# Kernel optimization log

Hardware: AMD Instinct MI355X
Metric: run time of the kernel (lower is better)

## Reference

```python
import jax, jax.numpy as jnp
import numpy as np

SCALE = 100.0        # self.scale in the torch module
NUM_PIDS = 20000     # upper bound on particle_id values (fill_max)
N_HITS = 2_000_000
D_PARAMS = 8


def setup_inputs() -> dict:
    key = jax.random.key(0)
    ks = jax.random.split(key, 8)
    N, D = N_HITS, D_PARAMS
    return {
        "W": jax.random.uniform(ks[0], (N,), jnp.float32),
        "beta": jax.random.uniform(ks[1], (N,), jnp.float32, 1e-4, 1.0 - 1e-4),
        "H": jax.random.normal(ks[2], (N, D), jnp.float32),
        "pred": jax.random.normal(ks[3], (N, D), jnp.float32),
        "Y": jax.random.normal(ks[4], (N,), jnp.float32),
        "particle_id": jax.random.randint(ks[5], (N,), 0, NUM_PIDS, dtype=jnp.int32),
        "track_params": jax.random.normal(ks[6], (N, D), jnp.float32),
        "reconstructable": jnp.ones((N,), jnp.int32),
    }


def reference(W, beta, H, pred, Y, particle_id, track_params, reconstructable):
    # mask = reconstructable > 0; masked-out hits are routed to segment 0 (noise),
    # which is excluded from the per-pid loop, so math matches boolean indexing.
    valid = reconstructable > 0
    seg = jnp.where(valid, particle_id, 0)

    # MSE per hit: sum over param dim of squared error
    mse = jnp.sum(jnp.square(pred - track_params), axis=1)
    mse = jnp.where(valid, mse, 0.0)

    # In 'efficiency' mode the torch loop computes, per pid p:
    #   xi_p = M * p, weight = 1/sum(xi_p), contrib = weight * sum(mse * xi_p)
    #         = sum(mse * M) / count(M)   (the pid factor cancels exactly)
    # i.e. a segment-mean of mse over hits of each nonzero pid, averaged over pids.
    sums = jax.ops.segment_sum(mse, seg, num_segments=NUM_PIDS)
    counts = jax.ops.segment_sum(valid.astype(jnp.float32), seg, num_segments=NUM_PIDS)

    present = (counts > 0) & (jnp.arange(NUM_PIDS) > 0)  # pids from torch.unique(pid>0)
    per_pid_mean = jnp.where(present, sums / jnp.where(counts > 0, counts, 1.0), 0.0)
    K = jnp.sum(present.astype(jnp.float32))
    return SCALE * jnp.sum(per_pid_mean) / K
```

## Files before the change

kernel.cpp:

```cpp
#include <hip/hip_runtime.h>
#include <stdint.h>

#define NUM_PIDS 20000
#define HBLK_MAX 128
#define NCH      8
#define FIXB     512.0f
#define FXMASK   0x1FFFFu


__global__ void zero_acc_kernel(float* __restrict__ acc) {
    if (threadIdx.x < 2) acc[threadIdx.x] = 0.0f;
}

__global__ void __launch_bounds__(256) mse_kernel(
        const float4* __restrict__ pred,
        const float4* __restrict__ track,
        const int* __restrict__ pid,
        const int* __restrict__ recon,
        unsigned int* __restrict__ packed,
        int nf ) {
    int t = blockIdx.x * 256 + threadIdx.x;
    int stride = gridDim.x * 256;
    for (; t < nf; t += stride) {
        float4 a = pred[t], b = track[t];
        float d0 = a.x - b.x, d1 = a.y - b.y;
        float d2 = a.z - b.z, d3 = a.w - b.w;
        float part = d0*d0 + d1*d1 + d2*d2 + d3*d3;
        float mse = part + __shfl_xor(part, 1);
        int hit = t >> 1;
        int p = pid[hit];
        int r = recon[hit];
        unsigned int fx = (unsigned int)fminf(mse * FIXB + 0.5f, 131071.0f);
        unsigned int out = (p > 0 && r > 0) ? (((unsigned int)p << 17) | fx) : 0u;
        if ((t & 1) == 0) packed[hit] = out;
    }
}

__global__ void __launch_bounds__(1024) hist_kernel(
        const uint4* __restrict__ packed4,
        unsigned int* __restrict__ tbl,
        int n4,
        const unsigned int* __restrict__ packed,
        int n) {
    __shared__ unsigned int bins[NUM_PIDS];
    for (int j = threadIdx.x; j < NUM_PIDS; j += 1024) bins[j] = 0u;
    __syncthreads();
    int t = blockIdx.x * 1024 + threadIdx.x;
    int stride = gridDim.x * 1024;
    for (; t < n4; t += stride) {
        uint4 v = packed4[t];
        unsigned int p;
        p = v.x >> 17; if (p) atomicAdd(&bins[p], (1u << 24) | (v.x & FXMASK));
        p = v.y >> 17; if (p) atomicAdd(&bins[p], (1u << 24) | (v.y & FXMASK));
        p = v.z >> 17; if (p) atomicAdd(&bins[p], (1u << 24) | (v.z & FXMASK));
        p = v.w >> 17; if (p) atomicAdd(&bins[p], (1u << 24) | (v.w & FXMASK));
    }
    for (int i = 4 * n4 + blockIdx.x * 1024 + threadIdx.x; i < n; i += stride) {
        unsigned int c = packed[i];
        unsigned int p = c >> 17;
        if (p) atomicAdd(&bins[p], (1u << 24) | (c & FXMASK));
    }
    __syncthreads();
    unsigned int* my = tbl + (size_t)blockIdx.x * NUM_PIDS;
    for (int j = threadIdx.x; j < NUM_PIDS; j += 1024) my[j] = bins[j];
}

__global__ void __launch_bounds__(256) reduce1_kernel(
        const unsigned int* __restrict__ tbl,
        unsigned long long* __restrict__ tmp,
        int nblk) {
    int p = blockIdx.x * 256 + threadIdx.x;
    int c = blockIdx.y;
    if (p >= NUM_PIDS) return;
    int cs = (nblk + NCH - 1) / NCH;
    int b0 = c * cs, b1 = min(nblk, b0 + cs);
    unsigned long long sfx = 0ULL, cnt = 0ULL;
    for (int b = b0; b < b1; ++b) {
        unsigned int v = tbl[(size_t)b * NUM_PIDS + p];
        sfx += (unsigned long long)(v & 0xFFFFFFu);
        cnt += (unsigned long long)(v >> 24);
    }
    tmp[(size_t)c * NUM_PIDS + p] = (cnt << 40) | sfx;
}

__global__ void __launch_bounds__(256) reduce2_kernel(
        const unsigned long long* __restrict__ tmp,
        float* __restrict__ acc) {
    int p = blockIdx.x * 256 + threadIdx.x;
    float mean = 0.0f, pres = 0.0f;
    if (p >= 1 && p < NUM_PIDS) {
        unsigned long long s = 0ULL;
        #pragma unroll
        for (int c = 0; c < NCH; ++c) s += tmp[(size_t)c * NUM_PIDS + p];
        unsigned long long cnt = s >> 40;
        if (cnt > 0) {
            double sum = (double)(s & ((1ULL << 40) - 1)) * (1.0 / 512.0);
            mean = (float)(sum / (double)cnt);
            pres = 1.0f;
        }
    }
    #pragma unroll
    for (int off = 32; off > 0; off >>= 1) {
        mean += __shfl_down(mean, off);
        pres += __shfl_down(pres, off);
    }
    __shared__ float smean[4], spres[4];
    int wave = threadIdx.x >> 6, lane = threadIdx.x & 63;
    if (lane == 0) { smean[wave] = mean; spres[wave] = pres; }
    __syncthreads();
    if (threadIdx.x == 0) {
        atomicAdd(&acc[0], smean[0] + smean[1] + smean[2] + smean[3]);
        atomicAdd(&acc[1], spres[0] + spres[1] + spres[2] + spres[3]);
    }
}

__global__ void final_kernel(const float* __restrict__ acc,
                             float* __restrict__ out) {
    if (threadIdx.x == 0 && blockIdx.x == 0) {
        float K = acc[1];
        out[0] = (K > 0.0f) ? (100.0f * acc[0] / K) : 0.0f;
    }
}

extern "C" void kernel_launch(void* const* d_in, const int* in_sizes, int n_in,
                              void* d_out, int out_size, void* d_ws, size_t ws_size,
                              hipStream_t stream) {
    const float* pred  = (const float*)d_in[3];
    const int*   pid   = (const int*)d_in[5];
    const float* track = (const float*)d_in[6];
    const int*   recon = (const int*)d_in[7];
    int n = in_sizes[5];

    size_t packed_bytes = (((size_t)n * 4) + 63) & ~(size_t)63;
    size_t tmp_bytes = (size_t)NCH * NUM_PIDS * 8;
    int hblk = 8;
    if (ws_size > packed_bytes + tmp_bytes + 64 + (size_t)NUM_PIDS * 4) {
        size_t cap = (ws_size - packed_bytes - tmp_bytes - 64) / ((size_t)NUM_PIDS * 4);
        hblk = (int)(cap < HBLK_MAX ? cap : HBLK_MAX);
        if (hblk < 1) hblk = 1;
    }

    unsigned int* packed = (unsigned int*)d_ws;
    unsigned int* tbl = (unsigned int*)((char*)d_ws + packed_bytes);
    unsigned long long* tmp =
        (unsigned long long*)((char*)tbl + (size_t)hblk * NUM_PIDS * 4);
    float* acc = (float*)((char*)tmp + tmp_bytes);

    zero_acc_kernel<<<1, 64, 0, stream>>>(acc);
    mse_kernel<<<2048, 256, 0, stream>>>((const float4*)pred, (const float4*)track,
                                         pid, recon, packed, 2 * n);
    hist_kernel<<<hblk, 1024, 0, stream>>>((const uint4*)packed, tbl, n / 4,
                                           packed, n);
    dim3 g1((NUM_PIDS + 255) / 256, NCH);
    reduce1_kernel<<<g1, 256, 0, stream>>>(tbl, tmp, hblk);
    reduce2_kernel<<<(NUM_PIDS + 255) / 256, 256, 0, stream>>>(tmp, acc);
    final_kernel<<<1, 64, 0, stream>>>(acc, (float*)d_out);
}
```

Measured before the change: 49.63 us.

## Double-buffer MSE loads through LDS with async global_load_lds

Rewrites the MSE pass so each block streams 256-hit chunks of pred and track directly into LDS using global_load_lds, double-buffered with explicit vmcnt waits. One thread now handles a whole hit, replacing the cross-lane shuffle and the half-idle stores. The grid is cut to 1280 persistent blocks. The aim is to keep more memory requests in flight on this bandwidth-bound stage. The cost is reliance on hand-written inline asm and exact wait counts, which are fragile if the compiler reorders loads.

Result: slower. 51.09 us (+2.9%).

```diff
diff --git a/kernel.cpp b/kernel.cpp
--- a/kernel.cpp
+++ b/kernel.cpp
@@ -6,34 +6,106 @@
 #define NCH      8
 #define FIXB     512.0f
 #define FXMASK   0x1FFFFu
+#define CHUNK    256
+#define MSE_NBLK 1280
 
 
 __global__ void zero_acc_kernel(float* __restrict__ acc) {
     if (threadIdx.x < 2) acc[threadIdx.x] = 0.0f;
 }
 
+__device__ __forceinline__ unsigned int pack_hit(unsigned int p, unsigned int r, float mse) {
+    unsigned int fx = (unsigned int)fminf(mse * FIXB + 0.5f, 131071.0f);
+    return ((int)p > 0 && (int)r > 0) ? ((p << 17) | fx) : 0u;
+}
+
+#define GLDS16(g, l) __builtin_amdgcn_global_load_lds( \
+    (const __attribute__((address_space(1))) void*)(g), \
+    (__attribute__((address_space(3))) void*)(l), 16, 0, 0)
+
+#define WAITV(N) do { \
+    asm volatile("s_waitcnt vmcnt(" #N ")" ::: "memory"); \
+    __builtin_amdgcn_sched_barrier(0); } while (0)
+
 __global__ void __launch_bounds__(256) mse_kernel(
-        const float4* __restrict__ pred,
-        const float4* __restrict__ track,
-        const int* __restrict__ pid,
-        const int* __restrict__ recon,
+        const char* __restrict__ predG,
+        const char* __restrict__ trackG,
+        const char* __restrict__ pidG,
+        const char* __restrict__ recG,
         unsigned int* __restrict__ packed,
-        int nf ) {
-    int t = blockIdx.x * 256 + threadIdx.x;
-    int stride = gridDim.x * 256;
-    for (; t < nf; t += stride) {
-        float4 a = pred[t], b = track[t];
-        float d0 = a.x - b.x, d1 = a.y - b.y;
-        float d2 = a.z - b.z, d3 = a.w - b.w;
-        float part = d0*d0 + d1*d1 + d2*d2 + d3*d3;
-        float mse = part + __shfl_xor(part, 1);
-        int hit = t >> 1;
-        int p = pid[hit];
-        int r = recon[hit];
-        unsigned int fx = (unsigned int)fminf(mse * FIXB + 0.5f, 131071.0f);
-        unsigned int out = (p > 0 && r > 0) ? (((unsigned int)p << 17) | fx) : 0u;
-        if ((t & 1) == 0) packed[hit] = out;
-    }
+        int n) {
+    __shared__ float4 P0[CHUNK * 2], T0[CHUNK * 2];
+    __shared__ float4 P1[CHUNK * 2], T1[CHUNK * 2];
+
+    const int w = threadIdx.x >> 6;
+    const int l = threadIdx.x & 63;
+    const long nfull = n / CHUNK;
+    const long stride = gridDim.x;
+
+#define STAGE(PB, TB, c, pReg, rReg) do { \
+        long base_ = (long)(c) * (CHUNK * 32) + (long)w * 2048; \
+        const char* gp_ = predG + base_ + (long)l * 16; \
+        const char* gt_ = trackG + base_ + (long)l * 16; \
+        char* dp_ = (char*)(PB) + w * 2048; \
+        char* dt_ = (char*)(TB) + w * 2048; \
+        GLDS16(gp_,        dp_); \
+        GLDS16(gp_ + 1024, dp_ + 1024); \
+        GLDS16(gt_,        dt_); \
+        GLDS16(gt_ + 1024, dt_ + 1024); \
+        long hit_ = (long)(c) * CHUNK + w * 64 + l; \
+        asm volatile("global_load_dword %0, %2, off\n\t" \
+                     "global_load_dword %1, %3, off" \
+                     : "=&v"(pReg), "=&v"(rReg) \
+                     : "v"(pidG + hit_ * 4), "v"(recG + hit_ * 4) \
+                     : "memory"); \
+    } while (0)
+
+#define CONSUME(PB, TB, c, pReg, rReg) do { \
+        int h_ = w * 64 + l; \
+        float4 a0_ = (PB)[2 * h_], a1_ = (PB)[2 * h_ + 1]; \
+        float4 b0_ = (TB)[2 * h_], b1_ = (TB)[2 * h_ + 1]; \
+        float d0_ = a0_.x - b0_.x, d1_ = a0_.y - b0_.y; \
+        float d2_ = a0_.z - b0_.z, d3_ = a0_.w - b0_.w; \
+        float d4_ = a1_.x - b1_.x, d5_ = a1_.y - b1_.y; \
+        float d6_ = a1_.z - b1_.z, d7_ = a1_.w - b1_.w; \
+        float m_ = d0_*d0_ + d1_*d1_ + d2_*d2_ + d3_*d3_ \
+                 + d4_*d4_ + d5_*d5_ + d6_*d6_ + d7_*d7_; \
+        packed[(long)(c) * CHUNK + h_] = pack_hit(pReg, rReg, m_); \
+    } while (0)
+
+    long c = blockIdx.x;
+    unsigned int pA, rA, pB, rB;
+    if (c < nfull) {
+        STAGE(P0, T0, c, pA, rA);
+        for (;;) {
+            long cn = c + stride;
+            if (cn < nfull) { STAGE(P1, T1, cn, pB, rB); WAITV(6); }
+            else WAITV(0);
+            CONSUME(P0, T0, c, pA, rA);
+            if (cn >= nfull) break;
+            c = cn;
+            cn = c + stride;
+            if (cn < nfull) { STAGE(P0, T0, cn, pA, rA); WAITV(6); }
+            else WAITV(0);
+            CONSUME(P1, T1, c, pB, rB);
+            if (cn >= nfull) break;
+            c = cn;
+        }
+    }
+    if (blockIdx.x == 0) {
+        for (long h = nfull * CHUNK + threadIdx.x; h < n; h += 256) {
+            const float4* pa = (const float4*)(predG + h * 32);
+            const float4* pb = (const float4*)(trackG + h * 32);
+            float4 a0 = pa[0], a1 = pa[1], b0 = pb[0], b1 = pb[1];
+            float d0 = a0.x-b0.x, d1 = a0.y-b0.y, d2 = a0.z-b0.z, d3 = a0.w-b0.w;
+            float d4 = a1.x-b1.x, d5 = a1.y-b1.y, d6 = a1.z-b1.z, d7 = a1.w-b1.w;
+            float m = d0*d0+d1*d1+d2*d2+d3*d3 + d4*d4+d5*d5+d6*d6+d7*d7;
+            packed[h] = pack_hit(((const unsigned int*)pidG)[h],
+                                 ((const unsigned int*)recG)[h], m);
+        }
+    }
+#undef STAGE
+#undef CONSUME
 }
 
 __global__ void __launch_bounds__(1024) hist_kernel(
@@ -125,10 +197,10 @@
 extern "C" void kernel_launch(void* const* d_in, const int* in_sizes, int n_in,
                               void* d_out, int out_size, void* d_ws, size_t ws_size,
                               hipStream_t stream) {
-    const float* pred  = (const float*)d_in[3];
-    const int*   pid   = (const int*)d_in[5];
-    const float* track = (const float*)d_in[6];
-    const int*   recon = (const int*)d_in[7];
+    const char* pred  = (const char*)d_in[3];
+    const char* pid   = (const char*)d_in[5];
+    const char* track = (const char*)d_in[6];
+    const char* recon = (const char*)d_in[7];
     int n = in_sizes[5];
 
     size_t packed_bytes = (((size_t)n * 4) + 63) & ~(size_t)63;
@@ -146,9 +218,13 @@
         (unsigned long long*)((char*)tbl + (size_t)hblk * NUM_PIDS * 4);
     float* acc = (float*)((char*)tmp + tmp_bytes);
 
+    int nb = MSE_NBLK;
+    long nfull = n / CHUNK;
+    if (nfull > 0 && nfull < nb) nb = (int)nfull;
+    if (nb < 1) nb = 1;
+
     zero_acc_kernel<<<1, 64, 0, stream>>>(acc);
-    mse_kernel<<<2048, 256, 0, stream>>>((const float4*)pred, (const float4*)track,
-                                         pid, recon, packed, 2 * n);
+    mse_kernel<<<nb, 256, 0, stream>>>(pred, track, pid, recon, packed, n);
     hist_kernel<<<hblk, 1024, 0, stream>>>((const uint4*)packed, tbl, n / 4,
                                            packed, n);
     dim3 g1((NUM_PIDS + 255) / 256, NCH);
```
